# Kernel tuning notes

Hardware: AMD Instinct MI355X
Metric: run time of the kernel (lower is better)

The kernel has to match this reference:

```python
import jax, jax.numpy as jnp
import numpy as np

D_MODEL = 2048
NUM_HEADS = 16
HEAD_DIM = D_MODEL // NUM_HEADS
D_FF = 8192
EPS = 1e-6


def rmsnorm(x, w):
    return x * jax.lax.rsqrt(jnp.mean(x * x, axis=-1, keepdims=True) + EPS) * w


def setup_inputs() -> dict:
    key = jax.random.key(0)
    ks = jax.random.split(key, 8)
    B, S, D = 2, 2048, D_MODEL
    s = lambda d: 1.0 / np.sqrt(d)
    return {
        "x": jax.random.normal(ks[0], (B, S, D), dtype=jnp.float32),
        "w_qkv": jax.random.normal(ks[1], (D, 3 * D), dtype=jnp.float32) * s(D),
        "w_out": jax.random.normal(ks[2], (D, D), dtype=jnp.float32) * s(D),
        "w1": jax.random.normal(ks[3], (D, D_FF), dtype=jnp.float32) * s(D),
        "w2": jax.random.normal(ks[4], (D_FF, D), dtype=jnp.float32) * s(D_FF),
        "w3": jax.random.normal(ks[5], (D, D_FF), dtype=jnp.float32) * s(D),
        "g1": jnp.ones((D,), dtype=jnp.float32),
        "g2": jnp.ones((D,), dtype=jnp.float32),
    }


def attention(x, w_qkv, w_out):
    B, S, D = x.shape
    H, Hd = NUM_HEADS, HEAD_DIM
    qkv = (x @ w_qkv).reshape(B, S, 3, H, Hd)
    q = qkv[:, :, 0].transpose(0, 2, 1, 3)  # [B,H,S,Hd]
    k = qkv[:, :, 1].transpose(0, 2, 1, 3)
    v = qkv[:, :, 2].transpose(0, 2, 1, 3)
    scale = Hd ** -0.5
    attn = jnp.einsum("bhqd,bhkd->bhqk", q, k) * scale
    causal = jnp.tril(jnp.ones((S, S), dtype=bool))
    attn = jnp.where(causal, attn, -jnp.inf)
    attn = jax.nn.softmax(attn, axis=-1)
    out = jnp.einsum("bhqk,bhkd->bhqd", attn, v)
    out = out.transpose(0, 2, 1, 3).reshape(B, S, D)
    return out @ w_out


def ffn(x, w1, w2, w3):
    return (jax.nn.silu(x @ w1) * (x @ w3)) @ w2


def reference(x, w_qkv, w_out, w1, w2, w3, g1, g2):
    x = x + attention(rmsnorm(x, g1), w_qkv, w_out)
    return x + ffn(rmsnorm(x, g2), w1, w2, w3)
```

## Files before the change

### kernel.cpp

```cpp
#include <hip/hip_runtime.h>
#include <cstdint>
#include <cstddef>

typedef __bf16 bf16x8 __attribute__((ext_vector_type(8)));
typedef float f32x4 __attribute__((ext_vector_type(4)));

__device__ __forceinline__ void gl_lds16(const void* g, void* l) {
  __builtin_amdgcn_global_load_lds(
      (const __attribute__((address_space(1))) void*)g,
      (__attribute__((address_space(3))) void*)l, 16, 0, 0);
}

__global__ __launch_bounds__(256) void wconv_t_k(const float* __restrict__ W,
                                                 __bf16* __restrict__ WT,
                                                 int K, int N) {
  __shared__ float tile[32][33];
  const int c0 = blockIdx.x * 32, r0 = blockIdx.y * 32;
  const int tx = threadIdx.x & 31, ty = threadIdx.x >> 5;
#pragma unroll
  for (int i = 0; i < 32; i += 8)
    tile[ty + i][tx] = W[(size_t)(r0 + ty + i) * N + c0 + tx];
  __syncthreads();
#pragma unroll
  for (int i = 0; i < 32; i += 8)
    WT[(size_t)(c0 + ty + i) * K + r0 + tx] = (__bf16)tile[tx][ty + i];
}

__global__ __launch_bounds__(256) void rmsnorm_k(const float* __restrict__ x,
                                                 const float* __restrict__ g,
                                                 __bf16* __restrict__ out) {
  constexpr int D = 2048;
  const int row = blockIdx.x, t = threadIdx.x;
  const float4* xr = (const float4*)(x + (size_t)row * D);
  float4 a = xr[t * 2], b2 = xr[t * 2 + 1];
  float ss = a.x * a.x + a.y * a.y + a.z * a.z + a.w * a.w +
             b2.x * b2.x + b2.y * b2.y + b2.z * b2.z + b2.w * b2.w;
#pragma unroll
  for (int d = 1; d < 64; d <<= 1) ss += __shfl_xor(ss, d, 64);
  __shared__ float red[4];
  if ((t & 63) == 0) red[t >> 6] = ss;
  __syncthreads();
  float rs = rsqrtf((red[0] + red[1] + red[2] + red[3]) * (1.f / D) + 1e-6f);
  const float4* gr = (const float4*)g;
  float4 ga = gr[t * 2], gb = gr[t * 2 + 1];
  bf16x8 o8;
  o8[0] = (__bf16)(a.x * rs * ga.x);
  o8[1] = (__bf16)(a.y * rs * ga.y);
  o8[2] = (__bf16)(a.z * rs * ga.z);
  o8[3] = (__bf16)(a.w * rs * ga.w);
  o8[4] = (__bf16)(b2.x * rs * gb.x);
  o8[5] = (__bf16)(b2.y * rs * gb.y);
  o8[6] = (__bf16)(b2.z * rs * gb.z);
  o8[7] = (__bf16)(b2.w * rs * gb.w);
  *(bf16x8*)(out + (size_t)row * D + t * 8) = o8;
}

__global__ __launch_bounds__(256) void addred_k(const float* __restrict__ p0,
                                                const float* __restrict__ p1,
                                                const float* __restrict__ res,
                                                float* __restrict__ out, int n4) {
  int i = blockIdx.x * 256 + threadIdx.x;
  const int stride = gridDim.x * 256;
  for (; i < n4; i += stride) {
    float4 a = ((const float4*)p0)[i];
    float4 b = ((const float4*)p1)[i];
    float4 c = ((const float4*)res)[i];
    float4 o = {a.x + b.x + c.x, a.y + b.y + c.y, a.z + b.z + c.z, a.w + b.w + c.w};
    ((float4*)out)[i] = o;
  }
}

#define RD_A(BUF, HALF) do {                                        \
  const __bf16* aT_ = &As[BUF][0] + aoff + (HALF) * 4096;           \
  _Pragma("unroll")                                                 \
  for (int mi = 0; mi < 4; ++mi) {                                  \
    Ar[mi][0] = *(const bf16x8*)(aT_ + mi * 1024 + k0off);          \
    Ar[mi][1] = *(const bf16x8*)(aT_ + mi * 1024 + k1off);          \
  } } while (0)

#define RD_B(BUF, NH) do {                                          \
  const __bf16* bT_ = &Bs[BUF][0] + boff + (NH) * 2048;             \
  _Pragma("unroll")                                                 \
  for (int ni = 0; ni < 2; ++ni) {                                  \
    Br[NH][ni][0] = *(const bf16x8*)(bT_ + ni * 1024 + k0off);      \
    Br[NH][ni][1] = *(const bf16x8*)(bT_ + ni * 1024 + k1off);      \
  } } while (0)

#define MQ(MH, NH) do {                                             \
  _Pragma("unroll")                                                 \
  for (int mi = 0; mi < 4; ++mi) {                                  \
    _Pragma("unroll")                                               \
    for (int ni = 0; ni < 2; ++ni) {                                \
      f32x4& a_ = acc[(MH) * 4 + mi][(NH) * 2 + ni];                \
      a_ = __builtin_amdgcn_mfma_f32_16x16x32_bf16(Ar[mi][0], Br[NH][ni][0], a_, 0, 0, 0); \
      a_ = __builtin_amdgcn_mfma_f32_16x16x32_bf16(Ar[mi][1], Br[NH][ni][1], a_, 0, 0, 0); \
    } } } while (0)

#define PH_MID() do {                                               \
  __builtin_amdgcn_sched_barrier(0);                                \
  __builtin_amdgcn_s_barrier();                                     \
  asm volatile("s_waitcnt lgkmcnt(0)" ::: "memory");                \
  __builtin_amdgcn_sched_barrier(0);                                \
  __builtin_amdgcn_s_setprio(1);                                    \
} while (0)

#define PH_END(VM) do {                                             \
  __builtin_amdgcn_s_setprio(0);                                    \
  asm volatile("s_waitcnt vmcnt(" #VM ")" ::: "memory");            \
  __builtin_amdgcn_sched_barrier(0);                                \
  __builtin_amdgcn_s_barrier();                                     \
} while (0)

#define PH_END_NOVM() do {                                          \
  __builtin_amdgcn_s_setprio(0);                                    \
  __builtin_amdgcn_s_barrier();                                     \
} while (0)

#define KTILE(BUF, STG0, STG1, STG2, STG3, END0, END1, END3) do {   \
  RD_A(BUF, 0); RD_B(BUF, 0); STG0; PH_MID(); MQ(0, 0); END0;       \
  RD_B(BUF, 1);               STG1; PH_MID(); MQ(0, 1); END1;       \
  RD_A(BUF, 1);               STG2; PH_MID(); MQ(1, 1); PH_END_NOVM(); \
                              STG3; PH_MID(); MQ(1, 0); END3;       \
} while (0)

template <int MODE>
__global__ __launch_bounds__(512, 2) void gemm8_k(
    const __bf16* __restrict__ A, const __bf16* __restrict__ BT,
    const float* __restrict__ res, const __bf16* __restrict__ aux,
    void* __restrict__ Cout, int M, int N, int K, int lda, int cswz) {
  __shared__ alignas(16) __bf16 As[2][256 * 64];
  __shared__ alignas(16) __bf16 Bs[2][256 * 64];
  const int tid = threadIdx.x;
  const int lane = tid & 63, w = tid >> 6;
  const int wm = w >> 2, wn = w & 3;
  const int l15 = lane & 15, l16 = lane >> 4;

  const int nbx = gridDim.x, nby = gridDim.y;
  const int nwg = nbx * nby;
  const int bid = blockIdx.y * nbx + blockIdx.x;
  const int swz = (bid & 7) * (nwg >> 3) + (bid >> 3);
  int bx, by;
  if (cswz) { by = swz % nby; bx = swz / nby; }
  else      { bx = swz % nbx; by = swz / nbx; }
  const int m0 = by * 256, n0 = bx * 256;
  const int nkt = K >> 6;

  float* CoutF = (float*)Cout;
  if constexpr (MODE == 4) {
    const int z = blockIdx.z;
    A += (size_t)z * K;
    BT += (size_t)z * K;
    CoutF += (size_t)z * M * N;
  }

  const int srow = tid >> 3;
  const int scole = ((tid & 7) * 8) ^ ((srow & 7) << 3);
  const int brow_i = ((tid >> 8) << 6) + ((tid >> 3) & 31);

  auto stgA = [&](int t, int h) {
    if (t < nkt) {
      char* dst = (char*)(&As[t & 1][0]) + h * 8192 + tid * 16;
      const __bf16* src = A + (size_t)(m0 + h * 64 + srow) * lda + t * 64 + scole;
      gl_lds16(src, dst);
      gl_lds16(src + (size_t)128 * lda, dst + 16384);
    }
  };
  auto stgB = [&](int t, int h) {
    if (t < nkt) {
      const int r = h * 32 + brow_i;
      char* dst = (char*)(&Bs[t & 1][0]) + r * 128 + (tid & 7) * 16;
      const __bf16* src = BT + (size_t)(n0 + r) * lda + t * 64 + scole;
      gl_lds16(src, dst);
      gl_lds16(src + (size_t)128 * lda, dst + 16384);
    }
  };

  const int rswz = (l15 & 7) << 3;
  const int k0off = (l16 * 8) ^ rswz;
  const int k1off = (32 + l16 * 8) ^ rswz;
  const int aoff = (wm * 128 + l15) * 64;
  const int boff = (wn * 64 + l15) * 64;

  f32x4 acc[8][4] = {};
  bf16x8 Ar[4][2], Br[2][2][2];

  stgA(0, 0); stgB(0, 0); stgB(0, 1); stgA(0, 1);
  stgA(1, 0); stgB(1, 0);
  asm volatile("s_waitcnt vmcnt(8)" ::: "memory");
  __builtin_amdgcn_s_barrier();

  int t = 0;
  for (; t + 3 < nkt; t += 2) {
    KTILE(0, stgB(t + 1, 1), stgA(t + 1, 1), stgA(t + 2, 0), stgB(t + 2, 0),
          PH_END(8), PH_END(8), PH_END(8));
    KTILE(1, stgB(t + 2, 1), stgA(t + 2, 1), stgA(t + 3, 0), stgB(t + 3, 0),
          PH_END(8), PH_END(8), PH_END(8));
  }
  KTILE(0, stgB(t + 1, 1), stgA(t + 1, 1), (void)0, (void)0,
        PH_END(8), PH_END(8), PH_END(4));
  KTILE(1, (void)0, (void)0, (void)0, (void)0,
        PH_END(2), PH_END(0), __builtin_amdgcn_s_setprio(0));

#pragma unroll
  for (int m = 0; m < 8; ++m) {
    const int rowb = m0 + wm * 128 + m * 16 + l16 * 4;
#pragma unroll
    for (int n = 0; n < 4; ++n) {
      const int col = n0 + wn * 64 + n * 16 + l15;
#pragma unroll
      for (int r = 0; r < 4; ++r) {
        const size_t idx = (size_t)(rowb + r) * N + col;
        float v = acc[m][n][r];
        if constexpr (MODE == 1) {
          CoutF[idx] = v + res[idx];
        } else if constexpr (MODE == 2) {
          float s = v / (1.f + __expf(-v));
          ((__bf16*)Cout)[idx] = (__bf16)s;
        } else if constexpr (MODE == 3) {
          ((__bf16*)Cout)[idx] = (__bf16)(v * (float)aux[idx]);
        } else if constexpr (MODE == 4) {
          CoutF[idx] = v;
        } else {
          ((__bf16*)Cout)[idx] = (__bf16)v;
        }
      }
    }
  }
}

__global__ __launch_bounds__(256) void vtrans_k(const __bf16* __restrict__ qkv,
                                                __bf16* __restrict__ VT) {
  constexpr int S = 2048;
  __shared__ __bf16 tile[64][65];
  const int s0 = blockIdx.x * 64, d0 = blockIdx.y * 64;
  const int bh = blockIdx.z, b = bh >> 4, h = bh & 15;
  const int tx = threadIdx.x & 63, ty = threadIdx.x >> 6;
  const size_t vbase = ((size_t)b * S * 3 + 2) * 2048 + h * 128;
#pragma unroll
  for (int i = 0; i < 16; ++i) {
    int s = ty + i * 4;
    tile[s][tx] = qkv[vbase + (size_t)(s0 + s) * 6144 + d0 + tx];
  }
  __syncthreads();
  const size_t obase = ((size_t)bh * 128 + d0) * S + s0;
#pragma unroll
  for (int i = 0; i < 16; ++i) {
    int d = ty + i * 4;
    VT[obase + (size_t)d * S + tx] = tile[tx][d];
  }
}

__global__ __launch_bounds__(256) void attn_k(const __bf16* __restrict__ qkv,
                                              const __bf16* __restrict__ VT,
                                              __bf16* __restrict__ out) {
  constexpr int S = 2048;
  const int bid = blockIdx.x;
  const int qb = bid & 31;
  const int bh = bid >> 5;
  const int b = bh >> 4, h = bh & 15;
  const int q0 = qb * 64;
  const int tid = threadIdx.x, lane = tid & 63, w = tid >> 6;
  const int l15 = lane & 15, l16 = lane >> 4;

  __shared__ __bf16 Ks[64 * 128];
  __shared__ __bf16 Vs[128 * 64];
  __shared__ __bf16 Ps[4][16 * 72];

  const size_t qbase = (size_t)b * S * 6144 + h * 128;
  const size_t kbase = qbase + 2048;
  const size_t vtbase = (size_t)bh * 128 * 2048;

  bf16x8 qf[4];
  {
    const __bf16* qp = qkv + qbase + (size_t)(q0 + w * 16 + l15) * 6144 + l16 * 8;
#pragma unroll
    for (int kc = 0; kc < 4; ++kc) qf[kc] = *(const bf16x8*)(qp + kc * 32);
  }

  f32x4 o[8] = {};
  float mrow[4] = {-1e30f, -1e30f, -1e30f, -1e30f};
  float lrow[4] = {0.f, 0.f, 0.f, 0.f};
  const float sm = 0.08838834764831845f * 1.4426950408889634f;

  int ksrow[4], kscol[4], vsrow[4], vscol[4];
#pragma unroll
  for (int c = 0; c < 4; ++c) {
    int P = (c * 256 + tid) * 16;
    int kr = P >> 8;
    ksrow[c] = kr;
    kscol[c] = ((P & 255) ^ ((kr & 7) << 4)) >> 1;
    int vr = P >> 7;
    vsrow[c] = vr;
    vscol[c] = ((P & 127) ^ ((vr & 7) << 4)) >> 1;
  }
  const int fswz = (l15 & 7) << 3;
  const int qrow_abs = q0 + w * 16 + l16 * 4;

  for (int kt = 0; kt <= qb; ++kt) {
    const int k0 = kt * 64;
#pragma unroll
    for (int c = 0; c < 4; ++c) {
      int e = (c * 256 + tid) * 8;
      gl_lds16(qkv + kbase + (size_t)(k0 + ksrow[c]) * 6144 + kscol[c], &Ks[e]);
      gl_lds16(VT + vtbase + (size_t)vsrow[c] * 2048 + k0 + vscol[c], &Vs[e]);
    }
    __syncthreads();

    f32x4 s4[4];
#pragma unroll
    for (int f = 0; f < 4; ++f) {
      f32x4 accs = {};
#pragma unroll
      for (int kc = 0; kc < 4; ++kc) {
        bf16x8 kf = *(const bf16x8*)&Ks[(f * 16 + l15) * 128 + ((kc * 32 + l16 * 8) ^ fswz)];
        accs = __builtin_amdgcn_mfma_f32_16x16x32_bf16(qf[kc], kf, accs, 0, 0, 0);
      }
      s4[f] = accs;
    }

    float pm[4] = {-1e30f, -1e30f, -1e30f, -1e30f};
    float pvv[4][4];
#pragma unroll
    for (int f = 0; f < 4; ++f) {
      const int key = k0 + f * 16 + l15;
#pragma unroll
      for (int r = 0; r < 4; ++r) {
        float s = s4[f][r] * sm;
        if (key > qrow_abs + r) s = -1e30f;
        pvv[f][r] = s;
        pm[r] = fmaxf(pm[r], s);
      }
    }
#pragma unroll
    for (int d = 1; d < 16; d <<= 1) {
#pragma unroll
      for (int r = 0; r < 4; ++r) pm[r] = fmaxf(pm[r], __shfl_xor(pm[r], d, 64));
    }
    float fac[4], ts[4];
#pragma unroll
    for (int r = 0; r < 4; ++r) {
      float mn = fmaxf(mrow[r], pm[r]);
      fac[r] = exp2f(mrow[r] - mn);
      mrow[r] = mn;
      ts[r] = 0.f;
    }
#pragma unroll
    for (int f = 0; f < 4; ++f) {
#pragma unroll
      for (int r = 0; r < 4; ++r) {
        float p = exp2f(pvv[f][r] - mrow[r]);
        ts[r] += p;
        Ps[w][(l16 * 4 + r) * 72 + f * 16 + l15] = (__bf16)p;
      }
    }
#pragma unroll
    for (int d = 1; d < 16; d <<= 1) {
#pragma unroll
      for (int r = 0; r < 4; ++r) ts[r] += __shfl_xor(ts[r], d, 64);
    }
#pragma unroll
    for (int r = 0; r < 4; ++r) lrow[r] = lrow[r] * fac[r] + ts[r];
#pragma unroll
    for (int n = 0; n < 8; ++n) {
      o[n][0] *= fac[0];
      o[n][1] *= fac[1];
      o[n][2] *= fac[2];
      o[n][3] *= fac[3];
    }
#pragma unroll
    for (int kc = 0; kc < 2; ++kc) {
      bf16x8 pf = *(const bf16x8*)&Ps[w][l15 * 72 + kc * 32 + l16 * 8];
#pragma unroll
      for (int n = 0; n < 8; ++n) {
        bf16x8 vf = *(const bf16x8*)&Vs[(n * 16 + l15) * 64 + ((kc * 32 + l16 * 8) ^ fswz)];
        o[n] = __builtin_amdgcn_mfma_f32_16x16x32_bf16(pf, vf, o[n], 0, 0, 0);
      }
    }
    __syncthreads();
  }

  const int orow = b * S + q0 + w * 16 + l16 * 4;
#pragma unroll
  for (int r = 0; r < 4; ++r) {
    const float inv = 1.f / lrow[r];
#pragma unroll
    for (int n = 0; n < 8; ++n)
      out[(size_t)(orow + r) * 2048 + h * 128 + n * 16 + l15] = (__bf16)(o[n][r] * inv);
  }
}

extern "C" void kernel_launch(void* const* d_in, const int* in_sizes, int n_in,
                              void* d_out, int out_size, void* d_ws, size_t ws_size,
                              hipStream_t stream) {
  (void)in_sizes; (void)n_in; (void)out_size; (void)ws_size;
  const float* x = (const float*)d_in[0];
  const float* w_qkv = (const float*)d_in[1];
  const float* w_out = (const float*)d_in[2];
  const float* w1 = (const float*)d_in[3];
  const float* w2 = (const float*)d_in[4];
  const float* w3 = (const float*)d_in[5];
  const float* g1 = (const float*)d_in[6];
  const float* g2 = (const float*)d_in[7];
  char* ws = (char*)d_ws;

  constexpr int Mr = 4096, D = 2048, DFF = 8192, TD = 6144;

  __bf16* wqkvT = (__bf16*)(ws + 0);
  __bf16* w1T   = (__bf16*)(ws + 0);
  __bf16* woutT = (__bf16*)(ws + 33554432);
  __bf16* qkvb  = (__bf16*)(ws + 41943040);
  __bf16* w3T   = (__bf16*)(ws + 41943040);
  __bf16* w2T   = (__bf16*)(ws + 75497472);
  __bf16* VTb   = (__bf16*)(ws + 92274688);
  __bf16* xn    = (__bf16*)(ws + 109051904);
  __bf16* attn  = (__bf16*)(ws + 125829120);
  float*  hbuf  = (float*)(ws + 142606336);
  __bf16* gbuf  = (__bf16*)(ws + 176160768);
  float*  pO    = (float*)(ws + 176160768);
  float*  pW0   = (float*)(ws + 0);

  wconv_t_k<<<dim3(TD / 32, D / 32), 256, 0, stream>>>(w_qkv, wqkvT, D, TD);
  wconv_t_k<<<dim3(D / 32, D / 32), 256, 0, stream>>>(w_out, woutT, D, D);
  rmsnorm_k<<<Mr, 256, 0, stream>>>(x, g1, xn);
  gemm8_k<0><<<dim3(TD / 256, Mr / 256), 512, 0, stream>>>(xn, wqkvT, nullptr, nullptr, qkvb, Mr, TD, D, D, 1);
  vtrans_k<<<dim3(32, 2, 32), 256, 0, stream>>>(qkvb, VTb);
  attn_k<<<1024, 256, 0, stream>>>(qkvb, VTb, attn);
  gemm8_k<4><<<dim3(D / 256, Mr / 256, 2), 512, 0, stream>>>(attn, woutT, nullptr, nullptr, pO, Mr, D, D / 2, D, 0);
  addred_k<<<2048, 256, 0, stream>>>(pO, pO + (size_t)Mr * D, x, hbuf, Mr * D / 4);
  rmsnorm_k<<<Mr, 256, 0, stream>>>(hbuf, g2, xn);
  wconv_t_k<<<dim3(DFF / 32, D / 32), 256, 0, stream>>>(w1, w1T, D, DFF);
  wconv_t_k<<<dim3(DFF / 32, D / 32), 256, 0, stream>>>(w3, w3T, D, DFF);
  wconv_t_k<<<dim3(D / 32, DFF / 32), 256, 0, stream>>>(w2, w2T, DFF, D);
  gemm8_k<2><<<dim3(DFF / 256, Mr / 256), 512, 0, stream>>>(xn, w1T, nullptr, nullptr, gbuf, Mr, DFF, D, D, 1);
  gemm8_k<3><<<dim3(DFF / 256, Mr / 256), 512, 0, stream>>>(xn, w3T, nullptr, gbuf, gbuf, Mr, DFF, D, D, 1);
  gemm8_k<4><<<dim3(D / 256, Mr / 256, 2), 512, 0, stream>>>(gbuf, w2T, nullptr, nullptr, pW0, Mr, D, DFF / 2, DFF, 0);
  addred_k<<<2048, 256, 0, stream>>>(pW0, pW0 + (size_t)Mr * D, hbuf, (float*)d_out, Mr * D / 4);
}
```

Measured before the change: 853.2 us.

## Prefetch next K/V tile into registers and schedule longest causal blocks first

The attention kernel now loads the next K and V tiles into registers while the current tile's MFMAs run, then stores them to LDS after the barrier. This hides global-load latency that was previously exposed on every iteration. Block IDs are remapped so the causal query blocks with the most key tiles are dispatched first, and s_setprio raises wave priority around the MFMA sections. The cost is extra VGPRs for the prefetch buffers, which may lower occupancy.

```diff
diff --git a/kernel.cpp b/kernel.cpp
--- a/kernel.cpp
+++ b/kernel.cpp
@@ -255,8 +255,8 @@
                                               __bf16* __restrict__ out) {
   constexpr int S = 2048;
   const int bid = blockIdx.x;
-  const int qb = bid & 31;
-  const int bh = bid >> 5;
+  const int bh = (bid & 7) * 4 + ((bid >> 3) & 3);
+  const int qb = 31 - (bid >> 5);
   const int b = bh >> 4, h = bh & 15;
   const int q0 = qb * 64;
   const int tid = threadIdx.x, lane = tid & 63, w = tid >> 6;
@@ -296,17 +296,31 @@
   const int fswz = (l15 & 7) << 3;
   const int qrow_abs = q0 + w * 16 + l16 * 4;
 
+#pragma unroll
+  for (int c = 0; c < 4; ++c) {
+    int e = (c * 256 + tid) * 8;
+    gl_lds16(qkv + kbase + (size_t)ksrow[c] * 6144 + kscol[c], &Ks[e]);
+    gl_lds16(VT + vtbase + (size_t)vsrow[c] * 2048 + vscol[c], &Vs[e]);
+  }
+
   for (int kt = 0; kt <= qb; ++kt) {
     const int k0 = kt * 64;
-#pragma unroll
-    for (int c = 0; c < 4; ++c) {
-      int e = (c * 256 + tid) * 8;
-      gl_lds16(qkv + kbase + (size_t)(k0 + ksrow[c]) * 6144 + kscol[c], &Ks[e]);
-      gl_lds16(VT + vtbase + (size_t)vsrow[c] * 2048 + k0 + vscol[c], &Vs[e]);
-    }
     __syncthreads();
 
+    bf16x8 kreg[4], vreg[4];
+    const bool pf = kt < qb;
+    if (pf) {
+      const int kn = k0 + 64;
+#pragma unroll
+      for (int c = 0; c < 4; ++c)
+        kreg[c] = *(const bf16x8*)(qkv + kbase + (size_t)(kn + ksrow[c]) * 6144 + kscol[c]);
+#pragma unroll
+      for (int c = 0; c < 4; ++c)
+        vreg[c] = *(const bf16x8*)(VT + vtbase + (size_t)vsrow[c] * 2048 + kn + vscol[c]);
+    }
+
     f32x4 s4[4];
+    __builtin_amdgcn_s_setprio(1);
 #pragma unroll
     for (int f = 0; f < 4; ++f) {
       f32x4 accs = {};
@@ -317,6 +331,7 @@
       }
       s4[f] = accs;
     }
+    __builtin_amdgcn_s_setprio(0);
 
     float pm[4] = {-1e30f, -1e30f, -1e30f, -1e30f};
     float pvv[4][4];
@@ -367,16 +382,25 @@
       o[n][2] *= fac[2];
       o[n][3] *= fac[3];
     }
+    __builtin_amdgcn_s_setprio(1);
 #pragma unroll
     for (int kc = 0; kc < 2; ++kc) {
-      bf16x8 pf = *(const bf16x8*)&Ps[w][l15 * 72 + kc * 32 + l16 * 8];
+      bf16x8 pf2 = *(const bf16x8*)&Ps[w][l15 * 72 + kc * 32 + l16 * 8];
 #pragma unroll
       for (int n = 0; n < 8; ++n) {
         bf16x8 vf = *(const bf16x8*)&Vs[(n * 16 + l15) * 64 + ((kc * 32 + l16 * 8) ^ fswz)];
-        o[n] = __builtin_amdgcn_mfma_f32_16x16x32_bf16(pf, vf, o[n], 0, 0, 0);
+        o[n] = __builtin_amdgcn_mfma_f32_16x16x32_bf16(pf2, vf, o[n], 0, 0, 0);
       }
     }
+    __builtin_amdgcn_s_setprio(0);
     __syncthreads();
+
+    if (pf) {
+#pragma unroll
+      for (int c = 0; c < 4; ++c) *(bf16x8*)&Ks[(c * 256 + tid) * 8] = kreg[c];
+#pragma unroll
+      for (int c = 0; c < 4; ++c) *(bf16x8*)&Vs[(c * 256 + tid) * 8] = vreg[c];
+    }
   }
 
   const int orow = b * S + q0 + w * 16 + l16 * 4;
```

Measured after the change: 761.6 us. 1.12x faster.
